# Kernel optimization log

Measured on AMD Instinct MI355X. Metric: run time of the kernel, lower is better.

## Reference

```python
import jax, jax.numpy as jnp
import numpy as np

N_NODES = 100_000
N_EDGES = 1_600_000
F = 64      # in_features == hidden_features
DEPTH = 4
EPS = 1e-30


def setup_inputs() -> dict:
    key = jax.random.key(0)
    ks = jax.random.split(key, 16)
    s = 0.1  # weight scale
    return {
        "h": jax.random.normal(ks[0], (N_NODES, F), jnp.float32),
        "x": jax.random.normal(ks[1], (N_NODES, 3), jnp.float32),
        "src": jax.random.randint(ks[2], (N_EDGES,), 0, N_NODES, jnp.int32),
        "dst": jax.random.randint(ks[3], (N_EDGES,), 0, N_NODES, jnp.int32),
        "ew1": jax.random.normal(ks[4], (DEPTH, 2 * F + 1, F), jnp.float32) * s,
        "eb1": jnp.zeros((DEPTH, F), jnp.float32),
        "ew2": jax.random.normal(ks[5], (DEPTH, F, F), jnp.float32) * s,
        "eb2": jnp.zeros((DEPTH, F), jnp.float32),
        "nw1": jax.random.normal(ks[6], (DEPTH, 2 * F, F), jnp.float32) * s,
        "nb1": jnp.zeros((DEPTH, F), jnp.float32),
        "nw2": jax.random.normal(ks[7], (DEPTH, F, F), jnp.float32) * s,
        "nb2": jnp.zeros((DEPTH, F), jnp.float32),
        "cw1": jax.random.normal(ks[8], (DEPTH, F, F), jnp.float32) * s,
        "cb1": jnp.zeros((DEPTH, F), jnp.float32),
        "cw2": jax.random.normal(ks[9], (DEPTH, F, 1), jnp.float32) * s,
    }


def _egnn_layer(h, x, src, dst, ew1, eb1, ew2, eb2, nw1, nb1, nw2, nb2, cw1, cb1, cw2):
    n = h.shape[0]
    # per-edge gathers
    x_diff = x[src] - x[dst]                                   # [E, 3]
    radial = jnp.sum(x_diff * x_diff, axis=-1, keepdims=True)  # [E, 1]
    x_diff = x_diff / (jnp.sqrt(radial) + EPS)                 # normalized, DGL EGNNConv
    f = jnp.concatenate([h[src], h[dst], radial], axis=-1)     # [E, 2F+1]
    # edge MLP (SiLU x2)
    m = jax.nn.silu(f @ ew1 + eb1)
    m = jax.nn.silu(m @ ew2 + eb2)                             # msg_h, [E, F]
    # coord MLP -> scalar per edge, times normalized diff
    c = jax.nn.silu(m @ cw1 + cb1) @ cw2                       # [E, 1]
    msg_x = c * x_diff                                          # [E, 3]
    # scatter-sum to destination nodes
    h_neigh = jax.ops.segment_sum(m, dst, num_segments=n)      # [N, F]
    x_neigh = jax.ops.segment_sum(msg_x, dst, num_segments=n)  # [N, 3]
    # node update
    hn = jnp.concatenate([h, h_neigh], axis=-1)                # [N, 2F]
    h_new = jax.nn.silu(hn @ nw1 + nb1) @ nw2 + nb2
    x_new = x + x_neigh
    return h_new, x_new


def reference(h, x, src, dst, ew1, eb1, ew2, eb2, nw1, nb1, nw2, nb2, cw1, cb1, cw2):
    for d in range(DEPTH):
        h, x = _egnn_layer(h, x, src, dst,
                           ew1[d], eb1[d], ew2[d], eb2[d],
                           nw1[d], nb1[d], nw2[d], nb2[d],
                           cw1[d], cb1[d], cw2[d])
    return x
```

## Files before the change

### kernel.cpp

```cpp
#include <hip/hip_runtime.h>

#define N_NODES 100000
#define N_EDGES 1600000
#define F 64

static_assert(N_NODES % 16 == 0, "node groups exact");
static_assert(N_EDGES % 16 == 0, "edge groups exact");

using short8  = __attribute__((ext_vector_type(8))) short;
using f32x4   = __attribute__((ext_vector_type(4))) float;
using uint32x4 = __attribute__((ext_vector_type(4))) unsigned;

#define MSTR 68
#define EWAVES 8

#define NBLK_N ((N_NODES + 255) / 256)
#define NBLK_E (N_EDGES / 256)

__device__ __forceinline__ float silu_f(float v) {
    return v * __builtin_amdgcn_rcpf(1.0f + __expf(-v));
}

__device__ __forceinline__ short f2bf(float f) {
    unsigned u = __float_as_uint(f);
    unsigned r = (u + 0x7fffu + ((u >> 16) & 1u)) >> 16;
    return (short)r;
}
__device__ __forceinline__ float bf2f(short s) {
    return __uint_as_float(((unsigned)(unsigned short)s) << 16);
}

__device__ __forceinline__ unsigned cvt_pk_bf16(float a, float b) {
    unsigned r;
    asm("v_cvt_pk_bf16_f32 %0, %1, %2" : "=v"(r) : "v"(a), "v"(b));
    return r;
}

__device__ __forceinline__ void split8(const float* v, short8& h8, short8& l8) {
    unsigned hu[4], lu[4];
    #pragma unroll
    for (int p = 0; p < 4; ++p) {
        hu[p] = cvt_pk_bf16(v[2 * p], v[2 * p + 1]);
        const float r0 = v[2 * p]     - __uint_as_float(hu[p] << 16);
        const float r1 = v[2 * p + 1] - __uint_as_float(hu[p] & 0xffff0000u);
        lu[p] = cvt_pk_bf16(r0, r1);
    }
    h8 = __builtin_bit_cast(short8, (uint32x4){hu[0], hu[1], hu[2], hu[3]});
    l8 = __builtin_bit_cast(short8, (uint32x4){lu[0], lu[1], lu[2], lu[3]});
}


__global__ __launch_bounds__(256) void sort_zero(unsigned* __restrict__ cnt) {
    const int i = blockIdx.x * 256 + threadIdx.x;
    if (i < N_NODES) cnt[i] = 0u;
}

__global__ __launch_bounds__(256) void sort_hist(const int* __restrict__ dst,
                                                 unsigned* __restrict__ cnt) {
    const int e = blockIdx.x * 256 + threadIdx.x;
    atomicAdd(&cnt[dst[e]], 1u);
}

__global__ __launch_bounds__(256) void sort_psum(const unsigned* __restrict__ cnt,
                                                 unsigned* __restrict__ psum) {
    __shared__ unsigned ws[4];
    const int i = blockIdx.x * 256 + threadIdx.x;
    unsigned v = (i < N_NODES) ? cnt[i] : 0u;
    #pragma unroll
    for (int off = 1; off < 64; off <<= 1) v += __shfl_xor(v, off, 64);
    if ((threadIdx.x & 63) == 0) ws[threadIdx.x >> 6] = v;
    __syncthreads();
    if (threadIdx.x == 0) psum[blockIdx.x] = ws[0] + ws[1] + ws[2] + ws[3];
}

__global__ __launch_bounds__(64) void sort_scan(const unsigned* __restrict__ psum,
                                                unsigned* __restrict__ poff) {
    unsigned carry = 0u;
    const int t = threadIdx.x;
    for (int c = 0; c < NBLK_N; c += 64) {
        const int i = c + t;
        unsigned v = (i < NBLK_N) ? psum[i] : 0u;
        unsigned s = v;
        #pragma unroll
        for (int off = 1; off < 64; off <<= 1) {
            const unsigned u = __shfl_up(s, off, 64);
            if (t >= off) s += u;
        }
        if (i < NBLK_N) poff[i] = carry + s - v;
        carry += __shfl(s, 63, 64);
    }
}

__global__ __launch_bounds__(256) void sort_excl(const unsigned* __restrict__ cnt,
                                                 const unsigned* __restrict__ poff,
                                                 unsigned* __restrict__ cursor) {
    __shared__ unsigned ws[4];
    const int i = blockIdx.x * 256 + threadIdx.x;
    const unsigned v = (i < N_NODES) ? cnt[i] : 0u;
    unsigned s = v;
    #pragma unroll
    for (int off = 1; off < 64; off <<= 1) {
        const unsigned u = __shfl_up(s, off, 64);
        if ((threadIdx.x & 63) >= off) s += u;
    }
    if ((threadIdx.x & 63) == 63) ws[threadIdx.x >> 6] = s;
    __syncthreads();
    unsigned base = poff[blockIdx.x];
    const int w = threadIdx.x >> 6;
    #pragma unroll
    for (int k = 0; k < 3; ++k) if (k < w) base += ws[k];
    if (i < N_NODES) cursor[i] = base + s - v;
}

__global__ __launch_bounds__(256) void sort_scatter(const int* __restrict__ src,
                                                    const int* __restrict__ dst,
                                                    unsigned* __restrict__ cursor,
                                                    int* __restrict__ ssrc,
                                                    int* __restrict__ sdst) {
    const int e = blockIdx.x * 256 + threadIdx.x;
    const int d = dst[e];
    const unsigned p = atomicAdd(&cursor[d], 1u);
    ssrc[p] = src[e];
    sdst[p] = d;
}


__global__ __launch_bounds__(256, 2) void node_pre(
    const float* __restrict__ h, const float* __restrict__ ew1,
    float* __restrict__ A, float* __restrict__ B,
    float* __restrict__ h_neigh, float* __restrict__ x_neigh)
{
    __shared__ short8 wHb[16][64];
    __shared__ short8 wLb[16][64];
    const int tid = threadIdx.x;
    const int w = tid >> 6, lane = tid & 63;
    const int col = lane & 15, quad = lane >> 4;
    if (w == 0) {
        #pragma unroll
        for (int t = 0; t < 8; ++t)
            #pragma unroll
            for (int kb = 0; kb < 2; ++kb) {
                short8 hh, ll;
                #pragma unroll
                for (int j = 0; j < 8; ++j) {
                    const int k = (t >> 2) * 64 + kb * 32 + quad * 8 + j;
                    const float wv = ew1[k * 64 + (t & 3) * 16 + col];
                    const short hs = f2bf(wv);
                    hh[j] = hs; ll[j] = f2bf(wv - bf2f(hs));
                }
                wHb[t * 2 + kb][lane] = hh;
                wLb[t * 2 + kb][lane] = ll;
            }
    }
    __syncthreads();
    const int nwv = gridDim.x * 4;
    for (int g = blockIdx.x * 4 + w; g < N_NODES / 16; g += nwv) {
        asm volatile("" ::: "memory");
        const int n0 = g * 16;
        short8 ah[2], al[2];
        #pragma unroll
        for (int kb = 0; kb < 2; ++kb) {
            const f32x4* hp = (const f32x4*)(h + (size_t)(n0 + col) * 64 + kb * 32 + quad * 8);
            const f32x4 v0 = hp[0], v1 = hp[1];
            const float v[8] = {v0[0], v0[1], v0[2], v0[3], v1[0], v1[1], v1[2], v1[3]};
            split8(v, ah[kb], al[kb]);
        }
        #pragma unroll
        for (int t = 0; t < 8; ++t) {
            f32x4 z = {0.f, 0.f, 0.f, 0.f};
            #pragma unroll
            for (int kb = 0; kb < 2; ++kb) {
                const short8 Bh = wHb[t * 2 + kb][lane];
                const short8 Bl = wLb[t * 2 + kb][lane];
                z = __builtin_amdgcn_mfma_f32_16x16x32_bf16(ah[kb], Bh, z, 0, 0, 0);
                z = __builtin_amdgcn_mfma_f32_16x16x32_bf16(al[kb], Bh, z, 0, 0, 0);
                z = __builtin_amdgcn_mfma_f32_16x16x32_bf16(ah[kb], Bl, z, 0, 0, 0);
            }
            float* dstb = (t < 4) ? A : B;
            const int tt = t & 3;
            #pragma unroll
            for (int r = 0; r < 4; ++r)
                dstb[(size_t)(n0 + quad * 4 + r) * 64 + tt * 16 + col] = z[r];
        }
        {
            f32x4* hz = (f32x4*)(h_neigh + (size_t)n0 * 64 + lane * 16);
            const f32x4 zz = {0.f, 0.f, 0.f, 0.f};
            hz[0] = zz; hz[1] = zz; hz[2] = zz; hz[3] = zz;
        }
        if (lane < 48) x_neigh[n0 * 3 + lane] = 0.0f;
    }
}

__global__ __launch_bounds__(512, 2) void edge_mfma(
    const float* __restrict__ A, const float* __restrict__ B,
    const float* __restrict__ x,
    const int* __restrict__ ssrc, const int* __restrict__ sdst,
    const float* __restrict__ rw,  const float* __restrict__ eb1,
    const float* __restrict__ ew2, const float* __restrict__ eb2,
    const float* __restrict__ cw1, const float* __restrict__ cb1,
    const float* __restrict__ cw2,
    float* __restrict__ h_neigh, float* __restrict__ x_neigh)
{
    __shared__ float rwb[F], eb1b[F];
    __shared__ short8 wEhb[8][64];
    __shared__ short8 wElb[8][64];
    __shared__ short8 wChb[8][64];
    __shared__ short8 wClb[8][64];
    __shared__ unsigned mbuf_s[EWAVES][16 * MSTR];
    __shared__ float cbuf_s[EWAVES][16];
    __shared__ float xbuf_s[EWAVES][48];
    const int tid = threadIdx.x;
    const int w = tid >> 6, lane = tid & 63;
    const int col = lane & 15, quad = lane >> 4;
    if (tid < 64) rwb[tid] = rw[tid];
    else if (tid < 128) eb1b[tid - 64] = eb1[tid - 64];

    if (w == 0) {
        #pragma unroll
        for (int t = 0; t < 4; ++t)
            #pragma unroll
            for (int kb = 0; kb < 2; ++kb) {
                short8 weh, wch, wel, wcl;
                #pragma unroll
                for (int j = 0; j < 8; ++j) {
                    const int k = kb * 32 + quad * 8 + j;
                    const float we = ew2[k * 64 + t * 16 + col];
                    const float wc = cw1[k * 64 + t * 16 + col];
                    const short weh_s = f2bf(we);
                    const short wch_s = f2bf(wc);
                    weh[j] = weh_s; wch[j] = wch_s;
                    wel[j] = f2bf(we - bf2f(weh_s));
                    wcl[j] = f2bf(wc - bf2f(wch_s));
                }
                wEhb[t * 2 + kb][lane] = weh;
                wElb[t * 2 + kb][lane] = wel;
                wChb[t * 2 + kb][lane] = wch;
                wClb[t * 2 + kb][lane] = wcl;
            }
    }
    __syncthreads();

    unsigned* mbuf = &mbuf_s[w][0];
    float* cbuf = &cbuf_s[w][0];
    float* xbuf = &xbuf_s[w][0];

    float eb2c[4], cb1c[4], cw2c[4];
    #pragma unroll
    for (int t = 0; t < 4; ++t) {
        eb2c[t] = eb2[t * 16 + col];
        cb1c[t] = cb1[t * 16 + col];
        cw2c[t] = cw2[t * 16 + col];
    }

    const int eL = lane / 3;
    const int cc = lane - eL * 3;
    const int nwv = gridDim.x * EWAVES;
    for (int g = blockIdx.x * EWAVES + w; g < N_EDGES / 16; g += nwv) {
        asm volatile("" ::: "memory");

        const int e0 = g * 16;
        const int sv = ssrc[e0 + col];
        const int dv = sdst[e0 + col];

        const f32x4* ap = (const f32x4*)(A + (size_t)sv * 64);
        const f32x4* bp = (const f32x4*)(B + (size_t)dv * 64);
        f32x4 ag[4], bg[4];
        ag[0] = ap[quad * 2];     ag[1] = ap[quad * 2 + 1];
        ag[2] = ap[8 + quad * 2]; ag[3] = ap[8 + quad * 2 + 1];
        bg[0] = bp[quad * 2];     bg[1] = bp[quad * 2 + 1];
        bg[2] = bp[8 + quad * 2]; bg[3] = bp[8 + quad * 2 + 1];

        const int ms = __shfl(sv, eL, 64);
        const int md = __shfl(dv, eL, 64);
        float xs = 0.0f;
        if (lane < 48) xs = x[ms * 3 + cc] - x[md * 3 + cc];
        const float xx = xs * xs;
        const int b3 = col * 3;
        const float radE = __shfl(xx, b3, 64) + __shfl(xx, b3 + 1, 64)
                         + __shfl(xx, b3 + 2, 64);
        const float rad_e = __shfl(radE, eL, 64);
        const float xdn = xs / (sqrtf(rad_e) + 1e-30f);
        if (lane < 48) xbuf[lane] = xdn;

        short8 m1h[2], m1l[2];
        const float* agf = (const float*)ag;
        const float* bgf = (const float*)bg;
        #pragma unroll
        for (int kb = 0; kb < 2; ++kb) {
            float v[8];
            #pragma unroll
            for (int j = 0; j < 8; ++j) {
                const int k = kb * 32 + quad * 8 + j;
                const float pre = agf[kb * 8 + j] + bgf[kb * 8 + j]
                                + radE * rwb[k] + eb1b[k];
                v[j] = silu_f(pre);
            }
            split8(v, m1h[kb], m1l[kb]);
        }

        f32x4 acc[4];
        #pragma unroll
        for (int t = 0; t < 4; ++t) {
            f32x4 z = {0.f, 0.f, 0.f, 0.f};
            #pragma unroll
            for (int kb = 0; kb < 2; ++kb) {
                const short8 Eh = wEhb[t * 2 + kb][lane];
                const short8 El = wElb[t * 2 + kb][lane];
                z = __builtin_amdgcn_mfma_f32_16x16x32_bf16(m1h[kb], Eh, z, 0, 0, 0);
                z = __builtin_amdgcn_mfma_f32_16x16x32_bf16(m1l[kb], Eh, z, 0, 0, 0);
                z = __builtin_amdgcn_mfma_f32_16x16x32_bf16(m1h[kb], El, z, 0, 0, 0);
            }
            acc[t] = z;
        }

        #pragma unroll
        for (int t = 0; t < 4; ++t) {
            float v[4];
            #pragma unroll
            for (int r = 0; r < 4; ++r) v[r] = silu_f(acc[t][r] + eb2c[t]);
            #pragma unroll
            for (int p = 0; p < 2; ++p) {
                const unsigned hu = cvt_pk_bf16(v[2 * p], v[2 * p + 1]);
                const float r0 = v[2 * p]     - __uint_as_float(hu << 16);
                const float r1 = v[2 * p + 1] - __uint_as_float(hu & 0xffff0000u);
                const unsigned lu = cvt_pk_bf16(r0, r1);
                const unsigned w0 = (hu << 16) | (lu & 0xffffu);
                const unsigned w1 = (hu & 0xffff0000u) | (lu >> 16);
                mbuf[(quad * 4 + 2 * p)     * MSTR + t * 16 + col] = w0;
                mbuf[(quad * 4 + 2 * p + 1) * MSTR + t * 16 + col] = w1;
            }
        }

        {
            float hacc = 0.0f;
            int prev = __builtin_amdgcn_readlane(dv, 0);
            bool first = true;
            #pragma unroll
            for (int e = 0; e < 16; ++e) {
                const int de = __builtin_amdgcn_readlane(dv, e);
                if (de != prev) {
                    float* p = &h_neigh[(size_t)prev * 64 + lane];
                    if (first) atomicAdd(p, hacc); else *p = hacc;
                    first = false;
                    hacc = 0.0f;
                    prev = de;
                }
                const unsigned u = mbuf[e * MSTR + lane];
                hacc += bf2f((short)(u >> 16)) + bf2f((short)(u & 0xffffu));
            }
            atomicAdd(&h_neigh[(size_t)prev * 64 + lane], hacc);
        }

        short8 mh[2], ml[2];
        #pragma unroll
        for (int kb = 0; kb < 2; ++kb) {
            const unsigned* mp = &mbuf[col * MSTR + kb * 32 + quad * 8];
            short8 h8, l8;
            #pragma unroll
            for (int j = 0; j < 8; ++j) {
                const unsigned u = mp[j];
                h8[j] = (short)(u >> 16);
                l8[j] = (short)(u & 0xffffu);
            }
            mh[kb] = h8; ml[kb] = l8;
        }

        f32x4 acc2[4];
        #pragma unroll
        for (int t = 0; t < 4; ++t) {
            f32x4 z = {0.f, 0.f, 0.f, 0.f};
            #pragma unroll
            for (int kb = 0; kb < 2; ++kb) {
                const short8 Ch = wChb[t * 2 + kb][lane];
                const short8 Cl = wClb[t * 2 + kb][lane];
                z = __builtin_amdgcn_mfma_f32_16x16x32_bf16(mh[kb], Ch, z, 0, 0, 0);
                z = __builtin_amdgcn_mfma_f32_16x16x32_bf16(ml[kb], Ch, z, 0, 0, 0);
                z = __builtin_amdgcn_mfma_f32_16x16x32_bf16(mh[kb], Cl, z, 0, 0, 0);
            }
            acc2[t] = z;
        }

        float part[4] = {0.f, 0.f, 0.f, 0.f};
        #pragma unroll
        for (int t = 0; t < 4; ++t)
            #pragma unroll
            for (int r = 0; r < 4; ++r)
                part[r] = fmaf(silu_f(acc2[t][r] + cb1c[t]), cw2c[t], part[r]);
        #pragma unroll
        for (int off = 8; off >= 1; off >>= 1)
            #pragma unroll
            for (int r = 0; r < 4; ++r)
                part[r] += __shfl_xor(part[r], off, 64);

        if (col == 0) {
            f32x4 cv = {part[0], part[1], part[2], part[3]};
            *(f32x4*)&cbuf[quad * 4] = cv;
        }

        if (lane < 3) {
            float xacc = 0.0f;
            int prev = __builtin_amdgcn_readlane(dv, 0);
            bool first = true;
            #pragma unroll
            for (int e = 0; e < 16; ++e) {
                const int de = __builtin_amdgcn_readlane(dv, e);
                if (de != prev) {
                    float* p = &x_neigh[(size_t)prev * 3 + lane];
                    if (first) atomicAdd(p, xacc); else *p = xacc;
                    first = false;
                    xacc = 0.0f;
                    prev = de;
                }
                xacc = fmaf(cbuf[e], xbuf[e * 3 + lane], xacc);
            }
            atomicAdd(&x_neigh[(size_t)prev * 3 + lane], xacc);
        }
    }
}

__global__ __launch_bounds__(256, 2) void node_post(
    const float* __restrict__ h, const float* __restrict__ hng,
    const float* __restrict__ nw1, const float* __restrict__ nb1,
    const float* __restrict__ nw2, const float* __restrict__ nb2,
    const float* __restrict__ x_in, const float* __restrict__ xng,
    float* __restrict__ h_out, float* __restrict__ x_out)
{
    __shared__ short8 w1h[16][64], w1l[16][64];
    __shared__ short8 w2h[8][64],  w2l[8][64];
    __shared__ unsigned mbuf_s[4][16 * MSTR];
    const int tid = threadIdx.x;
    const int w = tid >> 6, lane = tid & 63;
    const int col = lane & 15, quad = lane >> 4;
    if (w == 0) {
        #pragma unroll
        for (int t = 0; t < 4; ++t) {
            #pragma unroll
            for (int kb = 0; kb < 4; ++kb) {
                short8 hh, ll;
                #pragma unroll
                for (int j = 0; j < 8; ++j) {
                    const int k = kb * 32 + quad * 8 + j;
                    const float wv = nw1[k * 64 + t * 16 + col];
                    const short hs = f2bf(wv);
                    hh[j] = hs; ll[j] = f2bf(wv - bf2f(hs));
                }
                w1h[t * 4 + kb][lane] = hh;
                w1l[t * 4 + kb][lane] = ll;
            }
            #pragma unroll
            for (int kb = 0; kb < 2; ++kb) {
                short8 hh, ll;
                #pragma unroll
                for (int j = 0; j < 8; ++j) {
                    const int k = kb * 32 + quad * 8 + j;
                    const float wv = nw2[k * 64 + t * 16 + col];
                    const short hs = f2bf(wv);
                    hh[j] = hs; ll[j] = f2bf(wv - bf2f(hs));
                }
                w2h[t * 2 + kb][lane] = hh;
                w2l[t * 2 + kb][lane] = ll;
            }
        }
    }
    __syncthreads();

    unsigned* mbuf = &mbuf_s[w][0];
    float b1c[4], b2c[4];
    #pragma unroll
    for (int t = 0; t < 4; ++t) {
        b1c[t] = nb1[t * 16 + col];
        b2c[t] = nb2[t * 16 + col];
    }

    const int nwv = gridDim.x * 4;
    for (int g = blockIdx.x * 4 + w; g < N_NODES / 16; g += nwv) {
        asm volatile("" ::: "memory");
        const int n0 = g * 16;
        short8 ah[4], al[4];
        #pragma unroll
        for (int kb = 0; kb < 4; ++kb) {
            const float* base = (kb < 2) ? h : hng;
            const f32x4* hp = (const f32x4*)(base + (size_t)(n0 + col) * 64
                                             + (kb & 1) * 32 + quad * 8);
            const f32x4 v0 = hp[0], v1 = hp[1];
            const float v[8] = {v0[0], v0[1], v0[2], v0[3], v1[0], v1[1], v1[2], v1[3]};
            split8(v, ah[kb], al[kb]);
        }

        #pragma unroll
        for (int t = 0; t < 4; ++t) {
            f32x4 z = {b1c[t], b1c[t], b1c[t], b1c[t]};
            #pragma unroll
            for (int kb = 0; kb < 4; ++kb) {
                const short8 Bh = w1h[t * 4 + kb][lane];
                const short8 Bl = w1l[t * 4 + kb][lane];
                z = __builtin_amdgcn_mfma_f32_16x16x32_bf16(ah[kb], Bh, z, 0, 0, 0);
                z = __builtin_amdgcn_mfma_f32_16x16x32_bf16(al[kb], Bh, z, 0, 0, 0);
                z = __builtin_amdgcn_mfma_f32_16x16x32_bf16(ah[kb], Bl, z, 0, 0, 0);
            }
            float v[4];
            #pragma unroll
            for (int r = 0; r < 4; ++r) v[r] = silu_f(z[r]);
            #pragma unroll
            for (int p = 0; p < 2; ++p) {
                const unsigned hu = cvt_pk_bf16(v[2 * p], v[2 * p + 1]);
                const float r0 = v[2 * p]     - __uint_as_float(hu << 16);
                const float r1 = v[2 * p + 1] - __uint_as_float(hu & 0xffff0000u);
                const unsigned lu = cvt_pk_bf16(r0, r1);
                const unsigned w0 = (hu << 16) | (lu & 0xffffu);
                const unsigned w1 = (hu & 0xffff0000u) | (lu >> 16);
                mbuf[(quad * 4 + 2 * p)     * MSTR + t * 16 + col] = w0;
                mbuf[(quad * 4 + 2 * p + 1) * MSTR + t * 16 + col] = w1;
            }
        }

        short8 mh[2], ml[2];
        #pragma unroll
        for (int kb = 0; kb < 2; ++kb) {
            const unsigned* mp = &mbuf[col * MSTR + kb * 32 + quad * 8];
            short8 h8, l8;
            #pragma unroll
            for (int j = 0; j < 8; ++j) {
                const unsigned u = mp[j];
                h8[j] = (short)(u >> 16);
                l8[j] = (short)(u & 0xffffu);
            }
            mh[kb] = h8; ml[kb] = l8;
        }

        #pragma unroll
        for (int t = 0; t < 4; ++t) {
            f32x4 z = {b2c[t], b2c[t], b2c[t], b2c[t]};
            #pragma unroll
            for (int kb = 0; kb < 2; ++kb) {
                const short8 Bh = w2h[t * 2 + kb][lane];
                const short8 Bl = w2l[t * 2 + kb][lane];
                z = __builtin_amdgcn_mfma_f32_16x16x32_bf16(mh[kb], Bh, z, 0, 0, 0);
                z = __builtin_amdgcn_mfma_f32_16x16x32_bf16(ml[kb], Bh, z, 0, 0, 0);
                z = __builtin_amdgcn_mfma_f32_16x16x32_bf16(mh[kb], Bl, z, 0, 0, 0);
            }
            #pragma unroll
            for (int r = 0; r < 4; ++r)
                h_out[(size_t)(n0 + quad * 4 + r) * 64 + t * 16 + col] = z[r];
        }

        if (lane < 48) x_out[n0 * 3 + lane] = x_in[n0 * 3 + lane] + xng[n0 * 3 + lane];
    }
}

__global__ __launch_bounds__(256) void x_finish(
    const float* __restrict__ x_in, const float* __restrict__ xng,
    float* __restrict__ x_out)
{
    const int i = blockIdx.x * 256 + threadIdx.x;
    if (i < N_NODES * 3) x_out[i] = x_in[i] + xng[i];
}

extern "C" void kernel_launch(void* const* d_in, const int* in_sizes, int n_in,
                              void* d_out, int out_size, void* d_ws, size_t ws_size,
                              hipStream_t stream) {
    const float* h_in0 = (const float*)d_in[0];
    const float* x_in0 = (const float*)d_in[1];
    const int*   src   = (const int*)d_in[2];
    const int*   dst   = (const int*)d_in[3];
    const float* ew1   = (const float*)d_in[4];
    const float* eb1   = (const float*)d_in[5];
    const float* ew2   = (const float*)d_in[6];
    const float* eb2   = (const float*)d_in[7];
    const float* nw1   = (const float*)d_in[8];
    const float* nb1   = (const float*)d_in[9];
    const float* nw2   = (const float*)d_in[10];
    const float* nb2   = (const float*)d_in[11];
    const float* cw1   = (const float*)d_in[12];
    const float* cb1   = (const float*)d_in[13];
    const float* cw2   = (const float*)d_in[14];
    float* out = (float*)d_out;

    const size_t NF = (size_t)N_NODES * F;
    float* A   = (float*)d_ws;
    float* Bm  = A + NF;
    float* hng = Bm + NF;
    float* h0  = hng + NF;
    float* h1  = h0 + NF;
    float* xw  = h1 + NF;
    float* xng = xw + (size_t)N_NODES * 3;
    unsigned* cnt    = (unsigned*)(xng + (size_t)N_NODES * 3);
    unsigned* cursor = cnt + N_NODES;
    unsigned* psum   = cursor + N_NODES;
    unsigned* poff   = psum + NBLK_N;
    int* ssrc = (int*)(poff + NBLK_N);
    int* sdst = ssrc + N_EDGES;

    sort_zero<<<NBLK_N, 256, 0, stream>>>(cnt);
    sort_hist<<<NBLK_E, 256, 0, stream>>>(dst, cnt);
    sort_psum<<<NBLK_N, 256, 0, stream>>>(cnt, psum);
    sort_scan<<<1, 64, 0, stream>>>(psum, poff);
    sort_excl<<<NBLK_N, 256, 0, stream>>>(cnt, poff, cursor);
    sort_scatter<<<NBLK_E, 256, 0, stream>>>(src, dst, cursor, ssrc, sdst);

    for (int d = 0; d < 4; ++d) {
        const float* hcur = (d == 0) ? h_in0 : ((d & 1) ? h0 : h1);
        float* hout = (d & 1) ? h1 : h0;
        const float* xcur = (d == 0) ? x_in0 : xw;
        node_pre<<<512, 256, 0, stream>>>(hcur, ew1 + (size_t)d * 129 * F,
                                          A, Bm, hng, xng);
        edge_mfma<<<512, 512, 0, stream>>>(A, Bm, xcur, ssrc, sdst,
            ew1 + (size_t)d * 129 * F + 128 * F, eb1 + d * F,
            ew2 + (size_t)d * F * F, eb2 + d * F,
            cw1 + (size_t)d * F * F, cb1 + d * F, cw2 + d * F,
            hng, xng);
        if (d < 3) {
            node_post<<<512, 256, 0, stream>>>(hcur, hng,
                nw1 + (size_t)d * 2 * F * F, nb1 + d * F,
                nw2 + (size_t)d * F * F, nb2 + d * F,
                xcur, xng, hout, xw);
        } else {
            x_finish<<<(N_NODES * 3 + 255) / 256, 256, 0, stream>>>(xcur, xng, out);
        }
    }
}
```

Baseline: 1.206 ms.

## Halve edge LDS staging buffer, split segment-sum by halves, parallelize weight prep

```diff
diff --git a/kernel.cpp b/kernel.cpp
--- a/kernel.cpp
+++ b/kernel.cpp
@@ -12,6 +12,7 @@
 using uint32x4 = __attribute__((ext_vector_type(4))) unsigned;
 
 #define MSTR 68
+#define MS2  36
 #define EWAVES 8
 
 #define NBLK_N ((N_NODES + 255) / 256)
@@ -135,22 +136,22 @@
     const int tid = threadIdx.x;
     const int w = tid >> 6, lane = tid & 63;
     const int col = lane & 15, quad = lane >> 4;
-    if (w == 0) {
-        #pragma unroll
-        for (int t = 0; t < 8; ++t)
-            #pragma unroll
-            for (int kb = 0; kb < 2; ++kb) {
-                short8 hh, ll;
-                #pragma unroll
-                for (int j = 0; j < 8; ++j) {
-                    const int k = (t >> 2) * 64 + kb * 32 + quad * 8 + j;
-                    const float wv = ew1[k * 64 + (t & 3) * 16 + col];
-                    const short hs = f2bf(wv);
-                    hh[j] = hs; ll[j] = f2bf(wv - bf2f(hs));
-                }
-                wHb[t * 2 + kb][lane] = hh;
-                wLb[t * 2 + kb][lane] = ll;
-            }
+    #pragma unroll
+    for (int tt = 0; tt < 2; ++tt) {
+        const int t = w * 2 + tt;
+        #pragma unroll
+        for (int kb = 0; kb < 2; ++kb) {
+            short8 hh, ll;
+            #pragma unroll
+            for (int j = 0; j < 8; ++j) {
+                const int k = (t >> 2) * 64 + kb * 32 + quad * 8 + j;
+                const float wv = ew1[k * 64 + (t & 3) * 16 + col];
+                const short hs = f2bf(wv);
+                hh[j] = hs; ll[j] = f2bf(wv - bf2f(hs));
+            }
+            wHb[t * 2 + kb][lane] = hh;
+            wLb[t * 2 + kb][lane] = ll;
+        }
     }
     __syncthreads();
     const int nwv = gridDim.x * 4;
@@ -206,7 +207,7 @@
     __shared__ short8 wElb[8][64];
     __shared__ short8 wChb[8][64];
     __shared__ short8 wClb[8][64];
-    __shared__ unsigned mbuf_s[EWAVES][16 * MSTR];
+    __shared__ unsigned mbuf_s[EWAVES][16 * MS2];
     __shared__ float cbuf_s[EWAVES][16];
     __shared__ float xbuf_s[EWAVES][48];
     const int tid = threadIdx.x;
@@ -215,28 +216,24 @@
     if (tid < 64) rwb[tid] = rw[tid];
     else if (tid < 128) eb1b[tid - 64] = eb1[tid - 64];
 
-    if (w == 0) {
-        #pragma unroll
-        for (int t = 0; t < 4; ++t)
-            #pragma unroll
-            for (int kb = 0; kb < 2; ++kb) {
-                short8 weh, wch, wel, wcl;
-                #pragma unroll
-                for (int j = 0; j < 8; ++j) {
-                    const int k = kb * 32 + quad * 8 + j;
-                    const float we = ew2[k * 64 + t * 16 + col];
-                    const float wc = cw1[k * 64 + t * 16 + col];
-                    const short weh_s = f2bf(we);
-                    const short wch_s = f2bf(wc);
-                    weh[j] = weh_s; wch[j] = wch_s;
-                    wel[j] = f2bf(we - bf2f(weh_s));
-                    wcl[j] = f2bf(wc - bf2f(wch_s));
-                }
-                wEhb[t * 2 + kb][lane] = weh;
-                wElb[t * 2 + kb][lane] = wel;
-                wChb[t * 2 + kb][lane] = wch;
-                wClb[t * 2 + kb][lane] = wcl;
-            }
+    {
+        const int t = w >> 1, kb = w & 1;
+        short8 weh, wch, wel, wcl;
+        #pragma unroll
+        for (int j = 0; j < 8; ++j) {
+            const int k = kb * 32 + quad * 8 + j;
+            const float we = ew2[k * 64 + t * 16 + col];
+            const float wc = cw1[k * 64 + t * 16 + col];
+            const short weh_s = f2bf(we);
+            const short wch_s = f2bf(wc);
+            weh[j] = weh_s; wch[j] = wch_s;
+            wel[j] = f2bf(we - bf2f(weh_s));
+            wcl[j] = f2bf(wc - bf2f(wch_s));
+        }
+        wEhb[t * 2 + kb][lane] = weh;
+        wElb[t * 2 + kb][lane] = wel;
+        wChb[t * 2 + kb][lane] = wch;
+        wClb[t * 2 + kb][lane] = wcl;
     }
     __syncthreads();
 
@@ -279,7 +276,7 @@
         const float radE = __shfl(xx, b3, 64) + __shfl(xx, b3 + 1, 64)
                          + __shfl(xx, b3 + 2, 64);
         const float rad_e = __shfl(radE, eL, 64);
-        const float xdn = xs / (sqrtf(rad_e) + 1e-30f);
+        const float xdn = xs * __builtin_amdgcn_rcpf(sqrtf(rad_e) + 1e-30f);
         if (lane < 48) xbuf[lane] = xdn;
 
         short8 m1h[2], m1l[2];
@@ -298,74 +295,73 @@
             split8(v, m1h[kb], m1l[kb]);
         }
 
-        f32x4 acc[4];
-        #pragma unroll
-        for (int t = 0; t < 4; ++t) {
-            f32x4 z = {0.f, 0.f, 0.f, 0.f};
-            #pragma unroll
-            for (int kb = 0; kb < 2; ++kb) {
-                const short8 Eh = wEhb[t * 2 + kb][lane];
-                const short8 El = wElb[t * 2 + kb][lane];
-                z = __builtin_amdgcn_mfma_f32_16x16x32_bf16(m1h[kb], Eh, z, 0, 0, 0);
-                z = __builtin_amdgcn_mfma_f32_16x16x32_bf16(m1l[kb], Eh, z, 0, 0, 0);
-                z = __builtin_amdgcn_mfma_f32_16x16x32_bf16(m1h[kb], El, z, 0, 0, 0);
-            }
-            acc[t] = z;
-        }
-
-        #pragma unroll
-        for (int t = 0; t < 4; ++t) {
-            float v[4];
-            #pragma unroll
-            for (int r = 0; r < 4; ++r) v[r] = silu_f(acc[t][r] + eb2c[t]);
-            #pragma unroll
-            for (int p = 0; p < 2; ++p) {
-                const unsigned hu = cvt_pk_bf16(v[2 * p], v[2 * p + 1]);
-                const float r0 = v[2 * p]     - __uint_as_float(hu << 16);
-                const float r1 = v[2 * p + 1] - __uint_as_float(hu & 0xffff0000u);
-                const unsigned lu = cvt_pk_bf16(r0, r1);
-                const unsigned w0 = (hu << 16) | (lu & 0xffffu);
-                const unsigned w1 = (hu & 0xffff0000u) | (lu >> 16);
-                mbuf[(quad * 4 + 2 * p)     * MSTR + t * 16 + col] = w0;
-                mbuf[(quad * 4 + 2 * p + 1) * MSTR + t * 16 + col] = w1;
-            }
-        }
-
-        {
-            float hacc = 0.0f;
-            int prev = __builtin_amdgcn_readlane(dv, 0);
-            bool first = true;
-            #pragma unroll
-            for (int e = 0; e < 16; ++e) {
-                const int de = __builtin_amdgcn_readlane(dv, e);
-                if (de != prev) {
-                    float* p = &h_neigh[(size_t)prev * 64 + lane];
-                    if (first) atomicAdd(p, hacc); else *p = hacc;
-                    first = false;
-                    hacc = 0.0f;
-                    prev = de;
+        short8 mh[2], ml[2];
+        #pragma unroll
+        for (int ph = 0; ph < 2; ++ph) {
+            #pragma unroll
+            for (int tt = 0; tt < 2; ++tt) {
+                const int t = ph * 2 + tt;
+                f32x4 z = {0.f, 0.f, 0.f, 0.f};
+                #pragma unroll
+                for (int kb = 0; kb < 2; ++kb) {
+                    const short8 Eh = wEhb[t * 2 + kb][lane];
+                    const short8 El = wElb[t * 2 + kb][lane];
+                    z = __builtin_amdgcn_mfma_f32_16x16x32_bf16(m1h[kb], Eh, z, 0, 0, 0);
+                    z = __builtin_amdgcn_mfma_f32_16x16x32_bf16(m1l[kb], Eh, z, 0, 0, 0);
+                    z = __builtin_amdgcn_mfma_f32_16x16x32_bf16(m1h[kb], El, z, 0, 0, 0);
                 }
-                const unsigned u = mbuf[e * MSTR + lane];
-                hacc += bf2f((short)(u >> 16)) + bf2f((short)(u & 0xffffu));
-            }
-            atomicAdd(&h_neigh[(size_t)prev * 64 + lane], hacc);
-        }
-
-        short8 mh[2], ml[2];
-        #pragma unroll
-        for (int kb = 0; kb < 2; ++kb) {
-            const unsigned* mp = &mbuf[col * MSTR + kb * 32 + quad * 8];
-            short8 h8, l8;
-            #pragma unroll
-            for (int j = 0; j < 8; ++j) {
-                const unsigned u = mp[j];
-                h8[j] = (short)(u >> 16);
-                l8[j] = (short)(u & 0xffffu);
-            }
-            mh[kb] = h8; ml[kb] = l8;
-        }
-
-        f32x4 acc2[4];
+                float v[4];
+                #pragma unroll
+                for (int r = 0; r < 4; ++r) v[r] = silu_f(z[r] + eb2c[t]);
+                #pragma unroll
+                for (int p = 0; p < 2; ++p) {
+                    const unsigned hu = cvt_pk_bf16(v[2 * p], v[2 * p + 1]);
+                    const float r0 = v[2 * p]     - __uint_as_float(hu << 16);
+                    const float r1 = v[2 * p + 1] - __uint_as_float(hu & 0xffff0000u);
+                    const unsigned lu = cvt_pk_bf16(r0, r1);
+                    const unsigned w0 = (hu << 16) | (lu & 0xffffu);
+                    const unsigned w1 = (hu & 0xffff0000u) | (lu >> 16);
+                    mbuf[(quad * 4 + 2 * p)     * MS2 + tt * 16 + col] = w0;
+                    mbuf[(quad * 4 + 2 * p + 1) * MS2 + tt * 16 + col] = w1;
+                }
+            }
+
+            {
+                const unsigned* mp = &mbuf[col * MS2 + quad * 8];
+                short8 h8, l8;
+                #pragma unroll
+                for (int j = 0; j < 8; ++j) {
+                    const unsigned u = mp[j];
+                    h8[j] = (short)(u >> 16);
+                    l8[j] = (short)(u & 0xffffu);
+                }
+                mh[ph] = h8; ml[ph] = l8;
+            }
+
+            if ((lane >> 5) == ph) {
+                const int feat = (lane & 31) + ph * 32;
+                const int fcol = lane & 31;
+                float hacc = 0.0f;
+                int prev = __builtin_amdgcn_readlane(dv, 0);
+                bool first = true;
+                #pragma unroll
+                for (int e = 0; e < 16; ++e) {
+                    const int de = __builtin_amdgcn_readlane(dv, e);
+                    if (de != prev) {
+                        float* p = &h_neigh[(size_t)prev * 64 + feat];
+                        if (first) atomicAdd(p, hacc); else *p = hacc;
+                        first = false;
+                        hacc = 0.0f;
+                        prev = de;
+                    }
+                    const unsigned u = mbuf[e * MS2 + fcol];
+                    hacc += bf2f((short)(u >> 16)) + bf2f((short)(u & 0xffffu));
+                }
+                atomicAdd(&h_neigh[(size_t)prev * 64 + feat], hacc);
+            }
+        }
+
+        float part[4] = {0.f, 0.f, 0.f, 0.f};
         #pragma unroll
         for (int t = 0; t < 4; ++t) {
             f32x4 z = {0.f, 0.f, 0.f, 0.f};
@@ -377,15 +373,10 @@
                 z = __builtin_amdgcn_mfma_f32_16x16x32_bf16(ml[kb], Ch, z, 0, 0, 0);
                 z = __builtin_amdgcn_mfma_f32_16x16x32_bf16(mh[kb], Cl, z, 0, 0, 0);
             }
-            acc2[t] = z;
-        }
-
-        float part[4] = {0.f, 0.f, 0.f, 0.f};
-        #pragma unroll
-        for (int t = 0; t < 4; ++t)
             #pragma unroll
             for (int r = 0; r < 4; ++r)
-                part[r] = fmaf(silu_f(acc2[t][r] + cb1c[t]), cw2c[t], part[r]);
+                part[r] = fmaf(silu_f(z[r] + cb1c[t]), cw2c[t], part[r]);
+        }
         #pragma unroll
         for (int off = 8; off >= 1; off >>= 1)
             #pragma unroll
@@ -431,35 +422,33 @@
     const int tid = threadIdx.x;
     const int w = tid >> 6, lane = tid & 63;
     const int col = lane & 15, quad = lane >> 4;
-    if (w == 0) {
-        #pragma unroll
-        for (int t = 0; t < 4; ++t) {
-            #pragma unroll
-            for (int kb = 0; kb < 4; ++kb) {
-                short8 hh, ll;
-                #pragma unroll
-                for (int j = 0; j < 8; ++j) {
-                    const int k = kb * 32 + quad * 8 + j;
-                    const float wv = nw1[k * 64 + t * 16 + col];
-                    const short hs = f2bf(wv);
-                    hh[j] = hs; ll[j] = f2bf(wv - bf2f(hs));
-                }
-                w1h[t * 4 + kb][lane] = hh;
-                w1l[t * 4 + kb][lane] = ll;
-            }
-            #pragma unroll
-            for (int kb = 0; kb < 2; ++kb) {
-                short8 hh, ll;
-                #pragma unroll
-                for (int j = 0; j < 8; ++j) {
-                    const int k = kb * 32 + quad * 8 + j;
-                    const float wv = nw2[k * 64 + t * 16 + col];
-                    const short hs = f2bf(wv);
-                    hh[j] = hs; ll[j] = f2bf(wv - bf2f(hs));
-                }
-                w2h[t * 2 + kb][lane] = hh;
-                w2l[t * 2 + kb][lane] = ll;
-            }
+    {
+        const int t = w;
+        #pragma unroll
+        for (int kb = 0; kb < 4; ++kb) {
+            short8 hh, ll;
+            #pragma unroll
+            for (int j = 0; j < 8; ++j) {
+                const int k = kb * 32 + quad * 8 + j;
+                const float wv = nw1[k * 64 + t * 16 + col];
+                const short hs = f2bf(wv);
+                hh[j] = hs; ll[j] = f2bf(wv - bf2f(hs));
+            }
+            w1h[t * 4 + kb][lane] = hh;
+            w1l[t * 4 + kb][lane] = ll;
+        }
+        #pragma unroll
+        for (int kb = 0; kb < 2; ++kb) {
+            short8 hh, ll;
+            #pragma unroll
+            for (int j = 0; j < 8; ++j) {
+                const int k = kb * 32 + quad * 8 + j;
+                const float wv = nw2[k * 64 + t * 16 + col];
+                const short hs = f2bf(wv);
+                hh[j] = hs; ll[j] = f2bf(wv - bf2f(hs));
+            }
+            w2h[t * 2 + kb][lane] = hh;
+            w2l[t * 2 + kb][lane] = ll;
         }
     }
     __syncthreads();
@@ -604,7 +593,7 @@
         const float* xcur = (d == 0) ? x_in0 : xw;
         node_pre<<<512, 256, 0, stream>>>(hcur, ew1 + (size_t)d * 129 * F,
                                           A, Bm, hng, xng);
-        edge_mfma<<<512, 512, 0, stream>>>(A, Bm, xcur, ssrc, sdst,
+        edge_mfma<<<768, 512, 0, stream>>>(A, Bm, xcur, ssrc, sdst,
             ew1 + (size_t)d * 129 * F + 128 * F, eb1 + d * F,
             ew2 + (size_t)d * F * F, eb2 + d * F,
             cw1 + (size_t)d * F * F, cb1 + d * F, cw2 + d * F,
```

After: 1.256 ms. +4.1%, slower.
